# Kernel optimization log

Hardware: AMD Instinct MI355X
Metric: run time of the kernel (lower is better)

Reference implementation:

```python
import jax, jax.numpy as jnp
import numpy as np

B, T, D = 2, 2048, 2048
H = 16
DK = 64          # head_k_dim (key_dim = D*0.5 = 1024)
DV = 128         # head_v_dim (value_dim = D*1.0 = 2048)
R = 16           # gate_low_rank_dim
GLN = 16.0       # gate_logit_normalizer
C = 64           # chunk size
EPS = 1e-5


def setup_inputs() -> dict:
    key = jax.random.key(0)
    ks = jax.random.split(key, 12)
    s = 0.02
    return {
        "hidden_states": jax.random.normal(ks[0], (B, T, D), jnp.float32),
        "Wq": jax.random.normal(ks[1], (D, H * DK), jnp.float32) * s,
        "Wk": jax.random.normal(ks[2], (D, H * DK), jnp.float32) * s,
        "Wv": jax.random.normal(ks[3], (D, H * DV), jnp.float32) * s,
        "Wgk1": jax.random.normal(ks[4], (D, R), jnp.float32) * s,
        "Wgk2": jax.random.normal(ks[5], (R, H * DK), jnp.float32) * s,
        "bgk2": jnp.zeros((H * DK,), jnp.float32),
        "Wg1": jax.random.normal(ks[6], (D, R), jnp.float32) * s,
        "Wg2": jax.random.normal(ks[7], (R, H * DV), jnp.float32) * s,
        "bg2": jnp.zeros((H * DV,), jnp.float32),
        "Wo": jax.random.normal(ks[8], (H * DV, D), jnp.float32) * s,
        "gnorm_w": jnp.ones((DV,), jnp.float32),
    }


def _gla_chunk(q, k, v, gk):
    """Chunked gated linear attention.
    q,k,gk: [B,T,H,DK], v: [B,T,H,DV]. Recurrence:
    S_t = diag(exp(gk_t)) S_{t-1} + k_t v_t^T ; o_t = q_t @ S_t.
    """
    nC = T // C
    # [nC, B, H, C, d]
    def to_chunks(x):
        return x.reshape(B, nC, C, H, -1).transpose(1, 0, 3, 2, 4)
    qc, kc, vc, gkc = map(to_chunks, (q, k, v, gk))
    Gc = jnp.cumsum(gkc, axis=3)  # inclusive cumsum of log-decays within chunk
    tri = jnp.tril(jnp.ones((C, C), bool))

    def step(S, inp):
        q_c, k_c, v_c, G_c = inp  # [B,H,C,dk] / [B,H,C,dv]
        qg = q_c * jnp.exp(G_c)            # decays <= 0 within chunk -> safe
        kg = k_c * jnp.exp(-G_c)
        # inter-chunk: state contribution
        o = jnp.einsum('bhcd,bhde->bhce', qg, S)
        # intra-chunk causal attention with decay
        A = jnp.einsum('bhid,bhjd->bhij', qg, kg)
        A = jnp.where(tri, A, 0.0)
        o = o + jnp.einsum('bhij,bhje->bhie', A, v_c)
        # state update
        G_last = G_c[:, :, -1, :]                       # [B,H,dk]
        k_dec = k_c * jnp.exp(G_last[:, :, None, :] - G_c)
        S = S * jnp.exp(G_last)[:, :, :, None] + jnp.einsum('bhcd,bhce->bhde', k_dec, v_c)
        return S, o

    S0 = jnp.zeros((B, H, DK, DV), q.dtype)
    _, o = jax.lax.scan(step, S0, (qc, kc, vc, Gc))
    # [nC,B,H,C,dv] -> [B,T,H,dv]
    return o.transpose(1, 0, 3, 2, 4).reshape(B, T, H, DV)


def reference(hidden_states, Wq, Wk, Wv, Wgk1, Wgk2, bgk2, Wg1, Wg2, bg2, Wo, gnorm_w):
    hs = hidden_states
    q = jax.nn.silu(hs @ Wq).reshape(B, T, H, DK)
    k = jax.nn.silu(hs @ Wk).reshape(B, T, H, DK)
    v = jax.nn.silu(hs @ Wv).reshape(B, T, H, DV)
    gk = ((hs @ Wgk1) @ Wgk2 + bgk2).reshape(B, T, H, DK)
    gk = jax.nn.log_sigmoid(gk) / GLN
    q = q * (DK ** -0.5)  # fla default scale
    o = _gla_chunk(q, k, v, gk)  # [B,T,H,DV]
    # RMSNorm over head_v_dim
    o = o * jax.lax.rsqrt(jnp.mean(o * o, axis=-1, keepdims=True) + EPS) * gnorm_w
    g = ((hs @ Wg1) @ Wg2 + bg2).reshape(B, T, H, DV)
    o = o * jax.nn.sigmoid(g)
    return o.reshape(B, T, H * DV) @ Wo
```

## Files before the change

kernel.cpp:

```cpp
#include <hip/hip_runtime.h>
#include <cstdint>

#define Bq   2
#define Tq   2048
#define Dq   2048
#define Hq   16
#define DKq  64
#define DVq  128
#define Cq   64
#define NCq  32
#define Mq   4096
#define NBH  32

typedef _Float16 f16;
typedef f16 f16x4 __attribute__((ext_vector_type(4)));
typedef f16 f16x8 __attribute__((ext_vector_type(8)));
typedef float f32x4 __attribute__((ext_vector_type(4)));
typedef unsigned short u16;
typedef u16 u16x8 __attribute__((ext_vector_type(8)));

__device__ __forceinline__ void gl_lds16(const void* g, void* l) {
    __builtin_amdgcn_global_load_lds(
        (const __attribute__((address_space(1))) uint32_t*)g,
        (__attribute__((address_space(3))) uint32_t*)l, 16, 0, 0);
}

__global__ __launch_bounds__(256) void trans_all(const float* __restrict__ Wq,
                                                 const float* __restrict__ Wk,
                                                 const float* __restrict__ Wv,
                                                 const float* __restrict__ Wo,
                                                 f16* __restrict__ Qkv, f16* __restrict__ WoT) {
    __shared__ float sh[4096];
    int blk = blockIdx.x;
    int tid = threadIdx.x;
    const float* W; f16* Dh; int N, nt, kt; long rowoff;
    if (blk < 2048)      { W = Wq; N = 1024; int t = blk;        nt = t & 31; kt = t >> 5; Dh = Qkv; rowoff = 0; }
    else if (blk < 4096) { W = Wk; N = 1024; int t = blk - 2048; nt = t & 31; kt = t >> 5; Dh = Qkv; rowoff = 1024; }
    else if (blk < 8192) { W = Wv; N = 2048; int t = blk - 4096; nt = t & 63; kt = t >> 6; Dh = Qkv; rowoff = 2048; }
    else                 { W = Wo; N = 2048; int t = blk - 8192; nt = t & 63; kt = t >> 6; Dh = WoT; rowoff = 0; }
    int tx = tid & 31, ty = tid >> 5;
#pragma unroll
    for (int i = 0; i < 4; i++) {
        int k = kt * 32 + ty + i * 8;
        int n = nt * 32 + tx;
        sh[tx * 33 + ty + i * 8] = W[(long)k * N + n];
    }
    __syncthreads();
#pragma unroll
    for (int i = 0; i < 4; i++) {
        int n = nt * 32 + ty + i * 8;
        int k = kt * 32 + tx;
        Dh[(rowoff + n) * 2048L + k] = (f16)sh[(ty + i * 8) * 33 + tx];
    }
}

__global__ __launch_bounds__(256) void hs_conv(const float* __restrict__ in,
                                               f16* __restrict__ out) {
    long i = ((long)blockIdx.x * 256 + threadIdx.x) * 8;
    float4 a = *(const float4*)(in + i);
    float4 b = *(const float4*)(in + i + 4);
    f16x8 h;
    h[0] = (f16)a.x; h[1] = (f16)a.y; h[2] = (f16)a.z; h[3] = (f16)a.w;
    h[4] = (f16)b.x; h[5] = (f16)b.y; h[6] = (f16)b.z; h[7] = (f16)b.w;
    *(f16x8*)(out + i) = h;
}

__global__ __launch_bounds__(256) void lowrank_tg(const float* __restrict__ hs,
                                                  const float* __restrict__ Wgk1,
                                                  const float* __restrict__ Wg1,
                                                  float* __restrict__ t_gk,
                                                  float* __restrict__ t_g) {
    __shared__ float sW[512 * 32];
    int tid = threadIdx.x;
    int blk = blockIdx.x;
    int r = tid >> 4, seg = tid & 15;
    long row = (long)blk * 16 + r;
    float acc[32];
#pragma unroll
    for (int c = 0; c < 32; c++) acc[c] = 0.f;
    for (int kc = 0; kc < 2048; kc += 512) {
        __syncthreads();
#pragma unroll
        for (int i = 0; i < 16; i++) {
            int s = tid + i * 256;
            int k = s >> 3, q = s & 7;
            float4 w = (q < 4) ? *(const float4*)(Wgk1 + (long)(kc + k) * 16 + q * 4)
                               : *(const float4*)(Wg1  + (long)(kc + k) * 16 + (q - 4) * 4);
            int qs = q ^ ((k >> 5) & 7);
            *(float4*)&sW[k * 32 + qs * 4] = w;
        }
        __syncthreads();
        const float* hp = hs + row * 2048 + kc + seg * 32;
        int xr = seg & 7;
#pragma unroll
        for (int k4 = 0; k4 < 8; k4++) {
            float4 hv = *(const float4*)(hp + k4 * 4);
            float hvv[4] = {hv.x, hv.y, hv.z, hv.w};
#pragma unroll
            for (int u = 0; u < 4; u++) {
                int k = seg * 32 + k4 * 4 + u;
                const float* wr = &sW[k * 32];
#pragma unroll
                for (int q = 0; q < 8; q++) {
                    float4 wv = *(const float4*)(wr + ((q ^ xr) * 4));
                    acc[q * 4 + 0] += hvv[u] * wv.x;
                    acc[q * 4 + 1] += hvv[u] * wv.y;
                    acc[q * 4 + 2] += hvv[u] * wv.z;
                    acc[q * 4 + 3] += hvv[u] * wv.w;
                }
            }
        }
    }
#pragma unroll
    for (int c = 0; c < 32; c++) {
        acc[c] += __shfl_xor(acc[c], 1);
        acc[c] += __shfl_xor(acc[c], 2);
        acc[c] += __shfl_xor(acc[c], 4);
        acc[c] += __shfl_xor(acc[c], 8);
    }
    if (seg == 0) {
        float4 a;
        a.x = acc[0];  a.y = acc[1];  a.z = acc[2];  a.w = acc[3];  *(float4*)(t_gk + row * 16)     = a;
        a.x = acc[4];  a.y = acc[5];  a.z = acc[6];  a.w = acc[7];  *(float4*)(t_gk + row * 16 + 4) = a;
        a.x = acc[8];  a.y = acc[9];  a.z = acc[10]; a.w = acc[11]; *(float4*)(t_gk + row * 16 + 8) = a;
        a.x = acc[12]; a.y = acc[13]; a.z = acc[14]; a.w = acc[15]; *(float4*)(t_gk + row * 16 + 12)= a;
        a.x = acc[16]; a.y = acc[17]; a.z = acc[18]; a.w = acc[19]; *(float4*)(t_g + row * 16)      = a;
        a.x = acc[20]; a.y = acc[21]; a.z = acc[22]; a.w = acc[23]; *(float4*)(t_g + row * 16 + 4)  = a;
        a.x = acc[24]; a.y = acc[25]; a.z = acc[26]; a.w = acc[27]; *(float4*)(t_g + row * 16 + 8)  = a;
        a.x = acc[28]; a.y = acc[29]; a.z = acc[30]; a.w = acc[31]; *(float4*)(t_g + row * 16 + 12) = a;
    }
}

#define BARX()   asm volatile("s_barrier" ::: "memory")
#define LGKM0()  asm volatile("s_waitcnt lgkmcnt(0)" ::: "memory")
#define VMW8()   asm volatile("s_waitcnt vmcnt(8)" ::: "memory")

__global__ __launch_bounds__(512, 2) void gemm256(const f16* __restrict__ A,
                                                  const f16* __restrict__ Bt,
                                                  float* __restrict__ o0,
                                                  f16* __restrict__ h0,
                                                  f16* __restrict__ h1,
                                                  f16* __restrict__ h2,
                                                  int mode) {
    __shared__ __align__(16) f16 sA[2][16384];
    __shared__ __align__(16) f16 sB[2][16384];
    int tid = threadIdx.x;
    int wave = tid >> 6, lane = tid & 63;
    int quad = lane >> 4, l16 = lane & 15;
    int wm = wave >> 2, wn = wave & 3;

    int cpx = (int)gridDim.x >> 3;
    int wid = ((int)blockIdx.x & 7) * cpx + ((int)blockIdx.x >> 3);
    int bm = wid & 15, bn = wid >> 4;

    const f16* Ab = A  + (long)bm * 256 * 2048;
    const f16* Bb = Bt + (long)bn * 256 * 2048;

    int srow = tid >> 3;
    int gsrc = ((tid & 7) ^ (srow & 7)) * 8;
    const f16* Asrc = Ab + (long)srow * 2048 + gsrc;
    const f16* Bsrc = Bb + (long)srow * 2048 + gsrc;

#define STAGE(P, KT) do { \
    const f16* as_ = Asrc + (KT) * 64; \
    const f16* bs_ = Bsrc + (KT) * 64; \
    f16* la_ = &sA[P][tid * 8]; \
    f16* lb_ = &sB[P][tid * 8]; \
    _Pragma("unroll") \
    for (int q_ = 0; q_ < 4; q_++) gl_lds16(as_ + (long)q_ * 64 * 2048, la_ + q_ * 4096); \
    _Pragma("unroll") \
    for (int q_ = 0; q_ < 4; q_++) gl_lds16(bs_ + (long)q_ * 64 * 2048, lb_ + q_ * 4096); \
} while (0)

    int go0 = (quad ^ (l16 & 7)) * 8;
    int go1 = go0 ^ 32;
    const f16* aB0 = &sA[0][(wm * 128 + l16) * 64];
    const f16* aB1 = &sA[1][(wm * 128 + l16) * 64];
    const f16* bB0 = &sB[0][(wn * 64 + l16) * 64];
    const f16* bB1 = &sB[1][(wn * 64 + l16) * 64];

    f16x8 afr[4][2], bfr[2][2][2];
    f32x4 acc[8][4] = {};

#define LDA(PB, MH) do { \
    _Pragma("unroll") \
    for (int ii_ = 0; ii_ < 4; ii_++) { \
        afr[ii_][0] = *(const f16x8*)(PB + ((MH) * 4 + ii_) * 1024 + go0); \
        afr[ii_][1] = *(const f16x8*)(PB + ((MH) * 4 + ii_) * 1024 + go1); \
    } \
} while (0)

#define LDB(PB, NH) do { \
    _Pragma("unroll") \
    for (int jj_ = 0; jj_ < 2; jj_++) { \
        bfr[NH][jj_][0] = *(const f16x8*)(PB + ((NH) * 2 + jj_) * 1024 + go0); \
        bfr[NH][jj_][1] = *(const f16x8*)(PB + ((NH) * 2 + jj_) * 1024 + go1); \
    } \
} while (0)

#define QMFMA(MH, NH) do { \
    __builtin_amdgcn_s_setprio(1); \
    _Pragma("unroll") \
    for (int ii_ = 0; ii_ < 4; ii_++) \
    _Pragma("unroll") \
    for (int jj_ = 0; jj_ < 2; jj_++) { \
        acc[(MH)*4+ii_][(NH)*2+jj_] = __builtin_amdgcn_mfma_f32_16x16x32_f16(afr[ii_][0], bfr[NH][jj_][0], acc[(MH)*4+ii_][(NH)*2+jj_], 0, 0, 0); \
        acc[(MH)*4+ii_][(NH)*2+jj_] = __builtin_amdgcn_mfma_f32_16x16x32_f16(afr[ii_][1], bfr[NH][jj_][1], acc[(MH)*4+ii_][(NH)*2+jj_], 0, 0, 0); \
    } \
    __builtin_amdgcn_s_setprio(0); \
} while (0)

    STAGE(0, 0);
    STAGE(1, 1);
    VMW8();
    BARX();

#pragma unroll 1
    for (int it = 0; it < 16; it++) {
        int kt2 = 2 * it + 2; if (kt2 > 31) kt2 = 31;
        int kt3 = 2 * it + 3; if (kt3 > 31) kt3 = 31;
        LDA(aB0, 0); LDB(bB0, 0);
        BARX(); LGKM0(); QMFMA(0, 0); BARX();
        LDB(bB0, 1);
        BARX(); LGKM0(); QMFMA(0, 1); BARX();
        LDA(aB0, 1);
        BARX(); LGKM0(); QMFMA(1, 0); BARX();
        STAGE(0, kt2);
        VMW8();
        BARX(); QMFMA(1, 1); BARX();
        LDA(aB1, 0); LDB(bB1, 0);
        BARX(); LGKM0(); QMFMA(0, 0); BARX();
        LDB(bB1, 1);
        BARX(); LGKM0(); QMFMA(0, 1); BARX();
        LDA(aB1, 1);
        BARX(); LGKM0(); QMFMA(1, 0); BARX();
        STAGE(1, kt3);
        VMW8();
        BARX(); QMFMA(1, 1); BARX();
    }
    asm volatile("s_waitcnt vmcnt(0)" ::: "memory");

    long rb = (long)bm * 256 + wm * 128 + quad * 4;
    if (mode == 0) {
        long cbase = (long)bn * 256 + wn * 64 + l16;
#pragma unroll
        for (int i = 0; i < 8; i++)
#pragma unroll
            for (int j = 0; j < 4; j++)
#pragma unroll
                for (int r = 0; r < 4; r++)
                    o0[(rb + i * 16 + r) * 2048 + cbase + j * 16] = acc[i][j][r];
    } else {
        f16* dst; long cw, cb; float sc = 1.f;
        if (bn < 4)      { dst = h0; cw = 1024; cb = (long)bn * 256;       sc = 0.125f; }
        else if (bn < 8) { dst = h1; cw = 1024; cb = (long)(bn - 4) * 256; }
        else             { dst = h2; cw = 2048; cb = (long)(bn - 8) * 256; }
        long cbase = cb + wn * 64 + l16;
#pragma unroll
        for (int i = 0; i < 8; i++)
#pragma unroll
            for (int j = 0; j < 4; j++)
#pragma unroll
                for (int r = 0; r < 4; r++) {
                    float x = acc[i][j][r];
                    x = x / (1.f + __expf(-x)) * sc;
                    dst[(rb + i * 16 + r) * cw + cbase + j * 16] = (f16)x;
                }
    }
#undef STAGE
#undef LDA
#undef LDB
#undef QMFMA
}

__global__ __launch_bounds__(256) void vtrans(const u16* __restrict__ v,
                                              u16* __restrict__ vT) {
    __shared__ uint32_t su[128 * 65];
    int tid = threadIdx.x;
    int t0 = (blockIdx.x >> 5) * 128;
    int e0 = (blockIdx.x & 31) * 64;
#pragma unroll
    for (int i = 0; i < 4; i++) {
        int tr = i * 32 + (tid >> 3);
        int ec = (tid & 7) * 8;
        u16x8 g = *(const u16x8*)(v + (long)(t0 + tr) * 2048 + e0 + ec);
#pragma unroll
        for (int j = 0; j < 8; j++) su[tr * 65 + ec + j] = g[j];
    }
    __syncthreads();
#pragma unroll
    for (int i = 0; i < 2; i++) {
        int er = i * 32 + (tid >> 3);
        int tch = (tid & 7) * 16;
        u16x8 o0, o1;
#pragma unroll
        for (int j = 0; j < 8; j++) {
            o0[j] = (u16)su[(tch + j) * 65 + er];
            o1[j] = (u16)su[(tch + 8 + j) * 65 + er];
        }
        u16* dst = vT + (long)(e0 + er) * 4096 + t0 + tch;
        *(u16x8*)dst = o0;
        *(u16x8*)(dst + 8) = o1;
    }
}

__global__ __launch_bounds__(256) void gk_cum(const float* __restrict__ t_gk,
                                              const float* __restrict__ Wgk2,
                                              const float* __restrict__ bgk2,
                                              float* __restrict__ G,
                                              float* __restrict__ dec) {
    __shared__ float sT[1024];
    __shared__ float sW[1024];
    __shared__ float sb[64];
    __shared__ float sG[64 * 64];
    int blk = blockIdx.x;
    int c = blk & 31, h = (blk >> 5) & 15, b = blk >> 9;
    int tid = threadIdx.x;
    long rowbase = (long)b * Tq + c * 64;
    {
        int idx = tid * 4;
        *(float4*)&sT[idx] = *(const float4*)(t_gk + rowbase * 16 + idx);
        int rr = idx >> 6, dd = idx & 63;
        *(float4*)&sW[idx] = *(const float4*)(Wgk2 + rr * 1024 + h * 64 + dd);
    }
    if (tid < 64) sb[tid] = bgk2[h * 64 + tid];
    __syncthreads();
    int tquad = tid >> 4, dgrp = tid & 15;
    float4 bg4 = *(float4*)&sb[dgrp * 4];
#pragma unroll
    for (int j = 0; j < 4; j++) {
        int t = tquad * 4 + j;
        float4 z = bg4;
#pragma unroll
        for (int rr = 0; rr < 16; rr++) {
            float tv = sT[t * 16 + rr];
            float4 wv = *(float4*)&sW[rr * 64 + dgrp * 4];
            z.x += tv * wv.x; z.y += tv * wv.y; z.z += tv * wv.z; z.w += tv * wv.w;
        }
        float4 o;
        o.x = (fminf(z.x, 0.f) - log1pf(__expf(-fabsf(z.x)))) * 0.0625f;
        o.y = (fminf(z.y, 0.f) - log1pf(__expf(-fabsf(z.y)))) * 0.0625f;
        o.z = (fminf(z.z, 0.f) - log1pf(__expf(-fabsf(z.z)))) * 0.0625f;
        o.w = (fminf(z.w, 0.f) - log1pf(__expf(-fabsf(z.w)))) * 0.0625f;
        *(float4*)&sG[t * 64 + dgrp * 4] = o;
    }
    __syncthreads();
    if (tid < 64) {
        float run = 0.f;
        for (int t = 0; t < 64; t++) { run += sG[t * 64 + tid]; sG[t * 64 + tid] = run; }
        dec[blk * 64 + tid] = __expf(run);
    }
    __syncthreads();
    float* Gb = G + (long)blk * 4096;
#pragma unroll
    for (int i = 0; i < 4; i++) {
        int f = tid + i * 256;
        *(float4*)(Gb + f * 4) = *(float4*)&sG[f * 4];
    }
}

#define ST 68
__global__ __launch_bounds__(256) void gla_pass1(const f16* __restrict__ kbuf,
                                                 const f16* __restrict__ vh,
                                                 const float* __restrict__ G,
                                                 float* __restrict__ U) {
    __shared__ float sG[64 * ST];
    __shared__ float sK[64 * ST];
    int blk = blockIdx.x;
    int c = blk & 31, h = (blk >> 5) & 15, b = blk >> 9;
    int tid = threadIdx.x;
    long rowbase = (long)b * Tq + c * 64;
    const float* Gb = G + (long)blk * 4096;
#pragma unroll
    for (int i = 0; i < 4; i++) {
        int f = tid + i * 256;
        float4 v = *(const float4*)(Gb + f * 4);
        int t = f >> 4, d0 = (f & 15) * 4;
        *(float4*)&sG[t * ST + d0] = v;
    }
    __syncthreads();
#pragma unroll
    for (int i = 0; i < 16; i++) {
        int idx = tid + i * 256;
        int t = idx >> 6, d = idx & 63;
        float gl = sG[63 * ST + d];
        sK[t * ST + d] = (float)kbuf[(rowbase + t) * 1024 + h * 64 + d] * __expf(gl - sG[t * ST + d]);
    }
    __syncthreads();
    int ty = tid >> 4, tx = tid & 15;
    float acc[4][8] = {};
    const f16* vb = vh + rowbase * 2048 + h * 128 + tx * 8;
    for (int t = 0; t < 64; t++) {
        float kd[4];
        *(float4*)&kd[0] = *(float4*)&sK[t * ST + ty * 4];
        f16x8 vv = *(const f16x8*)(vb + (long)t * 2048);
        float ve[8];
#pragma unroll
        for (int e = 0; e < 8; e++) ve[e] = (float)vv[e];
#pragma unroll
        for (int r = 0; r < 4; r++)
#pragma unroll
            for (int e = 0; e < 8; e++) acc[r][e] += kd[r] * ve[e];
    }
    float* Ub = U + (long)blk * 8192;
#pragma unroll
    for (int r = 0; r < 4; r++) {
        int d = ty * 4 + r;
#pragma unroll
        for (int e8 = 0; e8 < 8; e8++)
            Ub[(tx * 8 + e8) * 64 + d] = acc[r][e8];
    }
}

__global__ __launch_bounds__(256) void gla_pass2(const float* __restrict__ U,
                                                 const float* __restrict__ dec,
                                                 f16* __restrict__ ShT) {
    int bh = blockIdx.x >> 2;
    int tid = threadIdx.x;
    int e = (blockIdx.x & 3) * 32 + (tid >> 3);
    int d0 = (tid & 7) * 8;
    float4 Sa = {0.f, 0.f, 0.f, 0.f}, Sb = {0.f, 0.f, 0.f, 0.f};
    for (int c = 0; c < NCq; c++) {
        long base = ((long)(bh * 32 + c) * 128 + e) * 64 + d0;
        float4 u0 = *(const float4*)(U + base);
        float4 u1 = *(const float4*)(U + base + 4);
        const float* dp = dec + (bh * 32 + c) * 64 + d0;
        float4 dc0 = *(const float4*)dp;
        float4 dc1 = *(const float4*)(dp + 4);
        f16x8 sh;
        sh[0] = (f16)Sa.x; sh[1] = (f16)Sa.y; sh[2] = (f16)Sa.z; sh[3] = (f16)Sa.w;
        sh[4] = (f16)Sb.x; sh[5] = (f16)Sb.y; sh[6] = (f16)Sb.z; sh[7] = (f16)Sb.w;
        *(f16x8*)(ShT + base) = sh;
        Sa.x = Sa.x * dc0.x + u0.x; Sa.y = Sa.y * dc0.y + u0.y;
        Sa.z = Sa.z * dc0.z + u0.z; Sa.w = Sa.w * dc0.w + u0.w;
        Sb.x = Sb.x * dc1.x + u1.x; Sb.y = Sb.y * dc1.y + u1.y;
        Sb.z = Sb.z * dc1.z + u1.z; Sb.w = Sb.w * dc1.w + u1.w;
    }
}

#define GRD(row, kslot) (((row) << 6) + ((((kslot) ^ ((row) & 7))) << 3))
__global__ __launch_bounds__(256) void gla_pass3(const f16* __restrict__ qb,
                                                 const f16* __restrict__ kb,
                                                 const float* __restrict__ G,
                                                 const float* __restrict__ t_g,
                                                 const float* __restrict__ Wg2,
                                                 const float* __restrict__ bg2,
                                                 const float* __restrict__ gnw,
                                                 const f16* __restrict__ ShT,
                                                 const f16* __restrict__ vT,
                                                 f16* __restrict__ Oh) {
    __shared__ __align__(16) f16 sQg[4096];
    __shared__ __align__(16) f16 sKg[4096];
    __shared__ __align__(16) f16 sAh[4096];
    __shared__ __align__(16) f16 sST[8192];
    __shared__ __align__(16) f16 sVT[8192];
    __shared__ float sWg[16 * 128];
    __shared__ float sbg[128];
    int blk = blockIdx.x;
    int c = blk & 31, h = (blk >> 5) & 15, b = blk >> 9;
    int tid = threadIdx.x;
    long rowbase = (long)b * Tq + c * 64;

#pragma unroll
    for (int i = 0; i < 4; i++) {
        int s = tid + i * 256;
        int e = s >> 3, gp = s & 7;
        int gl = gp ^ (e & 7);
        gl_lds16(ShT + (long)blk * 8192 + e * 64 + gl * 8, sST + s * 8);
        gl_lds16(vT + (long)(h * 128 + e) * 4096 + rowbase + gl * 8, sVT + s * 8);
    }
#pragma unroll
    for (int i = 0; i < 2; i++) {
        int idx = tid * 4 + i * 1024;
        int rr = idx >> 7, ee = idx & 127;
        *(float4*)&sWg[idx] = *(const float4*)(Wg2 + (long)rr * 2048 + h * 128 + ee);
    }
    if (tid < 128) sbg[tid] = bg2[h * 128 + tid];
#pragma unroll
    for (int i = 0; i < 4; i++) {
        int f = tid + i * 256;
        int t = f >> 4, gi = f & 15;
        float4 G4 = *(const float4*)(G + (long)blk * 4096 + f * 4);
        long gb = (rowbase + t) * 1024 + h * 64 + gi * 4;
        f16x4 q4 = *(const f16x4*)(qb + gb);
        f16x4 k4 = *(const f16x4*)(kb + gb);
        f16x4 qh, kh;
        float ex;
        ex = __expf(G4.x); qh[0] = (f16)((float)q4[0] * ex); kh[0] = (f16)((float)k4[0] / ex);
        ex = __expf(G4.y); qh[1] = (f16)((float)q4[1] * ex); kh[1] = (f16)((float)k4[1] / ex);
        ex = __expf(G4.z); qh[2] = (f16)((float)q4[2] * ex); kh[2] = (f16)((float)k4[2] / ex);
        ex = __expf(G4.w); qh[3] = (f16)((float)q4[3] * ex); kh[3] = (f16)((float)k4[3] / ex);
        int w = (t << 6) + ((((gi >> 1) ^ (t & 7))) << 3) + ((gi & 1) << 2);
        *(f16x4*)(sQg + w) = qh;
        *(f16x4*)(sKg + w) = kh;
    }
    __syncthreads();

    int wv = tid >> 6, lane = tid & 63;
    int quad = lane >> 4, l16 = lane & 15;
    int trow = wv * 16 + l16;

    f16x8 afq[2];
    afq[0] = *(const f16x8*)(sQg + GRD(trow, quad));
    afq[1] = *(const f16x8*)(sQg + GRD(trow, 4 + quad));
#pragma unroll
    for (int j4 = 0; j4 < 4; j4++) {
        int tc = j4 * 16 + l16;
        f16x8 bk0 = *(const f16x8*)(sKg + GRD(tc, quad));
        f16x8 bk1 = *(const f16x8*)(sKg + GRD(tc, 4 + quad));
        f32x4 ca = {};
        ca = __builtin_amdgcn_mfma_f32_16x16x32_f16(afq[0], bk0, ca, 0, 0, 0);
        ca = __builtin_amdgcn_mfma_f32_16x16x32_f16(afq[1], bk1, ca, 0, 0, 0);
#pragma unroll
        for (int r = 0; r < 4; r++) {
            int tr = wv * 16 + quad * 4 + r;
            int tcw = j4 * 16 + l16;
            f16 av = (tcw <= tr) ? (f16)ca[r] : (f16)0.f;
            sAh[(tr << 6) + ((((tcw >> 3) ^ (tr & 7))) << 3) + (tcw & 7)] = av;
        }
    }

    f16x8 afa[2];
    afa[0] = *(const f16x8*)(sAh + GRD(trow, quad));
    afa[1] = *(const f16x8*)(sAh + GRD(trow, 4 + quad));
    f32x4 acc[8];
#pragma unroll
    for (int et = 0; et < 8; et++) {
        int e = et * 16 + l16;
        f16x8 bs0 = *(const f16x8*)(sST + GRD(e, quad));
        f16x8 bs1 = *(const f16x8*)(sST + GRD(e, 4 + quad));
        f16x8 bv0 = *(const f16x8*)(sVT + GRD(e, quad));
        f16x8 bv1 = *(const f16x8*)(sVT + GRD(e, 4 + quad));
        f32x4 cc = {};
        cc = __builtin_amdgcn_mfma_f32_16x16x32_f16(afq[0], bs0, cc, 0, 0, 0);
        cc = __builtin_amdgcn_mfma_f32_16x16x32_f16(afq[1], bs1, cc, 0, 0, 0);
        cc = __builtin_amdgcn_mfma_f32_16x16x32_f16(afa[0], bv0, cc, 0, 0, 0);
        cc = __builtin_amdgcn_mfma_f32_16x16x32_f16(afa[1], bv1, cc, 0, 0, 0);
        acc[et] = cc;
    }

    float gw[8], bgv[8];
#pragma unroll
    for (int et = 0; et < 8; et++) {
        gw[et]  = gnw[et * 16 + l16];
        bgv[et] = sbg[et * 16 + l16];
    }
#pragma unroll
    for (int half = 0; half < 2; half++) {
        float tg[2][16];
#pragma unroll
        for (int rh = 0; rh < 2; rh++) {
            int t = wv * 16 + quad * 4 + half * 2 + rh;
            const float* tgp = t_g + (rowbase + t) * 16;
#pragma unroll
            for (int q4 = 0; q4 < 4; q4++)
                *(float4*)&tg[rh][q4 * 4] = *(const float4*)(tgp + q4 * 4);
        }
        float g[2][8];
#pragma unroll
        for (int rh = 0; rh < 2; rh++)
#pragma unroll
            for (int et = 0; et < 8; et++) g[rh][et] = bgv[et];
#pragma unroll
        for (int rr = 0; rr < 16; rr++) {
#pragma unroll
            for (int et = 0; et < 8; et++) {
                float wv_ = sWg[rr * 128 + et * 16 + l16];
                g[0][et] += tg[0][rr] * wv_;
                g[1][et] += tg[1][rr] * wv_;
            }
        }
#pragma unroll
        for (int rh = 0; rh < 2; rh++) {
            int r = half * 2 + rh;
            int t = wv * 16 + quad * 4 + r;
            float ss = 0.f;
#pragma unroll
            for (int et = 0; et < 8; et++) ss += acc[et][r] * acc[et][r];
            ss += __shfl_xor(ss, 1);
            ss += __shfl_xor(ss, 2);
            ss += __shfl_xor(ss, 4);
            ss += __shfl_xor(ss, 8);
            float scale = rsqrtf(ss * (1.f / 128.f) + 1e-5f);
            long off = (rowbase + t) * 2048 + h * 128 + l16;
#pragma unroll
            for (int et = 0; et < 8; et++) {
                float y = acc[et][r] * scale * gw[et] / (1.f + __expf(-g[rh][et]));
                Oh[off + et * 16] = (f16)y;
            }
        }
    }
}

extern "C" void kernel_launch(void* const* d_in, const int* in_sizes, int n_in,
                              void* d_out, int out_size, void* d_ws, size_t ws_size,
                              hipStream_t stream) {
    const float* hs   = (const float*)d_in[0];
    const float* Wq   = (const float*)d_in[1];
    const float* Wk   = (const float*)d_in[2];
    const float* Wv   = (const float*)d_in[3];
    const float* Wgk1 = (const float*)d_in[4];
    const float* Wgk2 = (const float*)d_in[5];
    const float* bgk2 = (const float*)d_in[6];
    const float* Wg1  = (const float*)d_in[7];
    const float* Wg2  = (const float*)d_in[8];
    const float* bg2  = (const float*)d_in[9];
    const float* Wo   = (const float*)d_in[10];
    const float* gnw  = (const float*)d_in[11];

    char* w = (char*)d_ws;
    auto alloc = [&](size_t bytes) {
        char* p = w; w += (bytes + 255) & ~size_t(255); return (void*)p;
    };
    f16*   Xh     = (f16*)  alloc((size_t)Mq * Dq * 2);
    f16*   WqkvT  = (f16*)  alloc((size_t)4224 * 2048 * 2);
    f16*   WoT    = (f16*)  alloc((size_t)2048 * 2048 * 2);
    f16*   qb     = (f16*)  alloc((size_t)Mq * 1024 * 2);
    f16*   kb     = (f16*)  alloc((size_t)Mq * 1024 * 2);
    f16*   vhb    = (f16*)  alloc((size_t)Mq * 2048 * 2);
    f16*   vTb    = (f16*)  alloc((size_t)Mq * 2048 * 2);
    float* t_gk   = (float*)alloc((size_t)Mq * 16 * 4);
    float* t_g    = (float*)alloc((size_t)Mq * 16 * 4);
    float* Ut     = (float*)alloc((size_t)NBH * NCq * 8192 * 4);
    f16*   ShT    = (f16*)  alloc((size_t)NBH * NCq * 8192 * 2);
    float* dec    = (float*)alloc((size_t)NBH * NCq * 64 * 4);
    float* Gbuf   = (float*)alloc((size_t)NBH * NCq * 4096 * 4);

    trans_all<<<12288, 256, 0, stream>>>(Wq, Wk, Wv, Wo, WqkvT, WoT);
    hs_conv<<<Mq * Dq / 2048, 256, 0, stream>>>(hs, Xh);
    lowrank_tg<<<256, 256, 0, stream>>>(hs, Wgk1, Wg1, t_gk, t_g);

    gemm256<<<256, 512, 0, stream>>>(Xh, WqkvT, nullptr, qb, kb, vhb, 1);
    vtrans<<<1024, 256, 0, stream>>>((const u16*)vhb, (u16*)vTb);

    gk_cum<<<NBH * NCq, 256, 0, stream>>>(t_gk, Wgk2, bgk2, Gbuf, dec);
    gla_pass1<<<NBH * NCq, 256, 0, stream>>>(kb, vhb, Gbuf, Ut);
    gla_pass2<<<NBH * 4, 256, 0, stream>>>(Ut, dec, ShT);
    gla_pass3<<<NBH * NCq, 256, 0, stream>>>(qb, kb, Gbuf, t_g, Wg2, bg2, gnw, ShT, vTb, Xh);

    gemm256<<<128, 512, 0, stream>>>(Xh, WoT, (float*)d_out, nullptr, nullptr, nullptr, 0);
}
```

Before: 415.2 us.

## Shrink GEMM tile to 128x256 with register double-buffered fragment pipeline

The gemm256 kernel's per-block tile changes from 256x256 to 128x256, which doubles the grid for both the QKV projection and the output projection. The output GEMM now launches 256 blocks instead of 128, filling more compute units. The inner loop is rebuilt so that LDS fragment reads for the next K-step are issued into a second register set while MFMAs run on the current one, with far fewer barriers per iteration. In exchange, each block reuses each B tile across fewer rows of A, so the kernel loads more data in total.

```diff
diff --git a/kernel.cpp b/kernel.cpp
--- a/kernel.cpp
+++ b/kernel.cpp
@@ -133,7 +133,7 @@
 
 #define BARX()   asm volatile("s_barrier" ::: "memory")
 #define LGKM0()  asm volatile("s_waitcnt lgkmcnt(0)" ::: "memory")
-#define VMW8()   asm volatile("s_waitcnt vmcnt(8)" ::: "memory")
+#define VMW6()   asm volatile("s_waitcnt vmcnt(6)" ::: "memory")
 
 __global__ __launch_bounds__(512, 2) void gemm256(const f16* __restrict__ A,
                                                   const f16* __restrict__ Bt,
@@ -142,8 +142,8 @@
                                                   f16* __restrict__ h1,
                                                   f16* __restrict__ h2,
                                                   int mode) {
-    __shared__ __align__(16) f16 sA[2][16384];
-    __shared__ __align__(16) f16 sB[2][16384];
+    __shared__ __align__(16) f16 sAb[16384];
+    __shared__ __align__(16) f16 sBb[32768];
     int tid = threadIdx.x;
     int wave = tid >> 6, lane = tid & 63;
     int quad = lane >> 4, l16 = lane & 15;
@@ -151,105 +151,90 @@
 
     int cpx = (int)gridDim.x >> 3;
     int wid = ((int)blockIdx.x & 7) * cpx + ((int)blockIdx.x >> 3);
-    int bm = wid & 15, bn = wid >> 4;
-
-    const f16* Ab = A  + (long)bm * 256 * 2048;
-    const f16* Bb = Bt + (long)bn * 256 * 2048;
+    int bm = wid & 31, bn = wid >> 5;
 
     int srow = tid >> 3;
     int gsrc = ((tid & 7) ^ (srow & 7)) * 8;
-    const f16* Asrc = Ab + (long)srow * 2048 + gsrc;
-    const f16* Bsrc = Bb + (long)srow * 2048 + gsrc;
+    const f16* Asrc = A  + ((long)bm * 128 + srow) * 2048 + gsrc;
+    const f16* Bsrc = Bt + ((long)bn * 256 + srow) * 2048 + gsrc;
 
 #define STAGE(P, KT) do { \
-    const f16* as_ = Asrc + (KT) * 64; \
-    const f16* bs_ = Bsrc + (KT) * 64; \
-    f16* la_ = &sA[P][tid * 8]; \
-    f16* lb_ = &sB[P][tid * 8]; \
     _Pragma("unroll") \
-    for (int q_ = 0; q_ < 4; q_++) gl_lds16(as_ + (long)q_ * 64 * 2048, la_ + q_ * 4096); \
+    for (int q_ = 0; q_ < 2; q_++) \
+        gl_lds16(Asrc + (KT) * 64 + (long)q_ * 64 * 2048, sAb + (P) * 8192 + tid * 8 + q_ * 4096); \
     _Pragma("unroll") \
-    for (int q_ = 0; q_ < 4; q_++) gl_lds16(bs_ + (long)q_ * 64 * 2048, lb_ + q_ * 4096); \
+    for (int q_ = 0; q_ < 4; q_++) \
+        gl_lds16(Bsrc + (KT) * 64 + (long)q_ * 64 * 2048, sBb + (P) * 16384 + tid * 8 + q_ * 4096); \
 } while (0)
 
     int go0 = (quad ^ (l16 & 7)) * 8;
     int go1 = go0 ^ 32;
-    const f16* aB0 = &sA[0][(wm * 128 + l16) * 64];
-    const f16* aB1 = &sA[1][(wm * 128 + l16) * 64];
-    const f16* bB0 = &sB[0][(wn * 64 + l16) * 64];
-    const f16* bB1 = &sB[1][(wn * 64 + l16) * 64];
-
-    f16x8 afr[4][2], bfr[2][2][2];
-    f32x4 acc[8][4] = {};
-
-#define LDA(PB, MH) do { \
-    _Pragma("unroll") \
-    for (int ii_ = 0; ii_ < 4; ii_++) { \
-        afr[ii_][0] = *(const f16x8*)(PB + ((MH) * 4 + ii_) * 1024 + go0); \
-        afr[ii_][1] = *(const f16x8*)(PB + ((MH) * 4 + ii_) * 1024 + go1); \
-    } \
+    const f16* pA0 = sAb + (wm * 64 + l16) * 64 + go0;
+    const f16* pA1 = sAb + (wm * 64 + l16) * 64 + go1;
+    const f16* pB0 = sBb + (wn * 64 + l16) * 64 + go0;
+    const f16* pB1 = sBb + (wn * 64 + l16) * 64 + go1;
+
+    f16x8 aX[4], bX[4], aY[4], bY[4];
+    f32x4 acc[4][4] = {};
+
+#define RDA(D, PTR, POFF) do { \
+    D[0] = *(const f16x8*)((PTR) + (POFF)); \
+    D[1] = *(const f16x8*)((PTR) + (POFF) + 1024); \
+    D[2] = *(const f16x8*)((PTR) + (POFF) + 2048); \
+    D[3] = *(const f16x8*)((PTR) + (POFF) + 3072); \
 } while (0)
 
-#define LDB(PB, NH) do { \
-    _Pragma("unroll") \
-    for (int jj_ = 0; jj_ < 2; jj_++) { \
-        bfr[NH][jj_][0] = *(const f16x8*)(PB + ((NH) * 2 + jj_) * 1024 + go0); \
-        bfr[NH][jj_][1] = *(const f16x8*)(PB + ((NH) * 2 + jj_) * 1024 + go1); \
-    } \
-} while (0)
-
-#define QMFMA(MH, NH) do { \
+#define MM(AS, BS) do { \
     __builtin_amdgcn_s_setprio(1); \
     _Pragma("unroll") \
-    for (int ii_ = 0; ii_ < 4; ii_++) \
+    for (int m_ = 0; m_ < 4; m_++) \
     _Pragma("unroll") \
-    for (int jj_ = 0; jj_ < 2; jj_++) { \
-        acc[(MH)*4+ii_][(NH)*2+jj_] = __builtin_amdgcn_mfma_f32_16x16x32_f16(afr[ii_][0], bfr[NH][jj_][0], acc[(MH)*4+ii_][(NH)*2+jj_], 0, 0, 0); \
-        acc[(MH)*4+ii_][(NH)*2+jj_] = __builtin_amdgcn_mfma_f32_16x16x32_f16(afr[ii_][1], bfr[NH][jj_][1], acc[(MH)*4+ii_][(NH)*2+jj_], 0, 0, 0); \
-    } \
+    for (int n_ = 0; n_ < 4; n_++) \
+        acc[m_][n_] = __builtin_amdgcn_mfma_f32_16x16x32_f16(AS[m_], BS[n_], acc[m_][n_], 0, 0, 0); \
     __builtin_amdgcn_s_setprio(0); \
 } while (0)
 
     STAGE(0, 0);
     STAGE(1, 1);
-    VMW8();
+    VMW6();
     BARX();
+    RDA(aX, pA0, 0); RDA(bX, pB0, 0);
 
 #pragma unroll 1
     for (int it = 0; it < 16; it++) {
-        int kt2 = 2 * it + 2; if (kt2 > 31) kt2 = 31;
-        int kt3 = 2 * it + 3; if (kt3 > 31) kt3 = 31;
-        LDA(aB0, 0); LDB(bB0, 0);
-        BARX(); LGKM0(); QMFMA(0, 0); BARX();
-        LDB(bB0, 1);
-        BARX(); LGKM0(); QMFMA(0, 1); BARX();
-        LDA(aB0, 1);
-        BARX(); LGKM0(); QMFMA(1, 0); BARX();
-        STAGE(0, kt2);
-        VMW8();
-        BARX(); QMFMA(1, 1); BARX();
-        LDA(aB1, 0); LDB(bB1, 0);
-        BARX(); LGKM0(); QMFMA(0, 0); BARX();
-        LDB(bB1, 1);
-        BARX(); LGKM0(); QMFMA(0, 1); BARX();
-        LDA(aB1, 1);
-        BARX(); LGKM0(); QMFMA(1, 0); BARX();
-        STAGE(1, kt3);
-        VMW8();
-        BARX(); QMFMA(1, 1); BARX();
+        int c2 = 2 * it + 2; if (c2 > 31) c2 = 31;
+        int c3 = 2 * it + 3; if (c3 > 31) c3 = 31;
+        RDA(aY, pA1, 0); RDA(bY, pB1, 0);
+        MM(aX, bX);
+        LGKM0();
+        BARX();
+        STAGE(0, c2);
+        VMW6();
+        BARX();
+        RDA(aX, pA0, 8192); RDA(bX, pB0, 16384);
+        MM(aY, bY);
+        RDA(aY, pA1, 8192); RDA(bY, pB1, 16384);
+        MM(aX, bX);
+        LGKM0();
+        BARX();
+        STAGE(1, c3);
+        VMW6();
+        BARX();
+        RDA(aX, pA0, 0); RDA(bX, pB0, 0);
+        MM(aY, bY);
     }
     asm volatile("s_waitcnt vmcnt(0)" ::: "memory");
 
-    long rb = (long)bm * 256 + wm * 128 + quad * 4;
+    long rb = (long)bm * 128 + wm * 64 + quad * 4;
     if (mode == 0) {
         long cbase = (long)bn * 256 + wn * 64 + l16;
 #pragma unroll
-        for (int i = 0; i < 8; i++)
-#pragma unroll
-            for (int j = 0; j < 4; j++)
+        for (int m = 0; m < 4; m++)
+#pragma unroll
+            for (int n = 0; n < 4; n++)
 #pragma unroll
                 for (int r = 0; r < 4; r++)
-                    o0[(rb + i * 16 + r) * 2048 + cbase + j * 16] = acc[i][j][r];
+                    o0[(rb + m * 16 + r) * 2048 + cbase + n * 16] = acc[m][n][r];
     } else {
         f16* dst; long cw, cb; float sc = 1.f;
         if (bn < 4)      { dst = h0; cw = 1024; cb = (long)bn * 256;       sc = 0.125f; }
@@ -257,20 +242,19 @@
         else             { dst = h2; cw = 2048; cb = (long)(bn - 8) * 256; }
         long cbase = cb + wn * 64 + l16;
 #pragma unroll
-        for (int i = 0; i < 8; i++)
-#pragma unroll
-            for (int j = 0; j < 4; j++)
+        for (int m = 0; m < 4; m++)
+#pragma unroll
+            for (int n = 0; n < 4; n++)
 #pragma unroll
                 for (int r = 0; r < 4; r++) {
-                    float x = acc[i][j][r];
+                    float x = acc[m][n][r];
                     x = x / (1.f + __expf(-x)) * sc;
-                    dst[(rb + i * 16 + r) * cw + cbase + j * 16] = (f16)x;
+                    dst[(rb + m * 16 + r) * cw + cbase + n * 16] = (f16)x;
                 }
     }
 #undef STAGE
-#undef LDA
-#undef LDB
-#undef QMFMA
+#undef RDA
+#undef MM
 }
 
 __global__ __launch_bounds__(256) void vtrans(const u16* __restrict__ v,
@@ -630,7 +614,7 @@
     hs_conv<<<Mq * Dq / 2048, 256, 0, stream>>>(hs, Xh);
     lowrank_tg<<<256, 256, 0, stream>>>(hs, Wgk1, Wg1, t_gk, t_g);
 
-    gemm256<<<256, 512, 0, stream>>>(Xh, WqkvT, nullptr, qb, kb, vhb, 1);
+    gemm256<<<512, 512, 0, stream>>>(Xh, WqkvT, nullptr, qb, kb, vhb, 1);
     vtrans<<<1024, 256, 0, stream>>>((const u16*)vhb, (u16*)vTb);
 
     gk_cum<<<NBH * NCq, 256, 0, stream>>>(t_gk, Wgk2, bgk2, Gbuf, dec);
@@ -638,5 +622,5 @@
     gla_pass2<<<NBH * 4, 256, 0, stream>>>(Ut, dec, ShT);
     gla_pass3<<<NBH * NCq, 256, 0, stream>>>(qb, kb, Gbuf, t_g, Wg2, bg2, gnw, ShT, vTb, Xh);
 
-    gemm256<<<128, 512, 0, stream>>>(Xh, WoT, (float*)d_out, nullptr, nullptr, nullptr, 0);
-}
+    gemm256<<<256, 512, 0, stream>>>(Xh, WoT, (float*)d_out, nullptr, nullptr, nullptr, 0);
+}
```

Measured after the change: 419.9 us. About the same (+1.1%).

## Split output GEMM into dedicated 128x256-tile kernel to fill all CUs

Applied to the files above, without the earlier changes.

The shared gemm256 kernel is split into a QKV-only variant and a new output-projection kernel, gemm128o, which uses 128x256 tiles. With smaller M tiles the output GEMM launches 256 blocks instead of 128, so more of the GPU's compute units have work for the final projection. The new kernel has its own double-buffered LDS pipeline with register ping-pong of MFMA operands and raised wave priority around the MFMA blocks. Each block now holds less output per unit of traffic, so A/B reuse is lower and more loads are issued per FLOP.

```diff
diff --git a/kernel.cpp b/kernel.cpp
--- a/kernel.cpp
+++ b/kernel.cpp
@@ -24,6 +24,11 @@
         (const __attribute__((address_space(1))) uint32_t*)g,
         (__attribute__((address_space(3))) uint32_t*)l, 16, 0, 0);
 }
+
+#define BARX()   asm volatile("s_barrier" ::: "memory")
+#define LGKM0()  asm volatile("s_waitcnt lgkmcnt(0)" ::: "memory")
+#define VMW8()   asm volatile("s_waitcnt vmcnt(8)" ::: "memory")
+#define VMW6()   asm volatile("s_waitcnt vmcnt(6)" ::: "memory")
 
 __global__ __launch_bounds__(256) void trans_all(const float* __restrict__ Wq,
                                                  const float* __restrict__ Wk,
@@ -131,17 +136,11 @@
     }
 }
 
-#define BARX()   asm volatile("s_barrier" ::: "memory")
-#define LGKM0()  asm volatile("s_waitcnt lgkmcnt(0)" ::: "memory")
-#define VMW8()   asm volatile("s_waitcnt vmcnt(8)" ::: "memory")
-
-__global__ __launch_bounds__(512, 2) void gemm256(const f16* __restrict__ A,
-                                                  const f16* __restrict__ Bt,
-                                                  float* __restrict__ o0,
-                                                  f16* __restrict__ h0,
-                                                  f16* __restrict__ h1,
-                                                  f16* __restrict__ h2,
-                                                  int mode) {
+__global__ __launch_bounds__(512, 2) void gemm256q(const f16* __restrict__ A,
+                                                   const f16* __restrict__ Bt,
+                                                   f16* __restrict__ h0,
+                                                   f16* __restrict__ h1,
+                                                   f16* __restrict__ h2) {
     __shared__ __align__(16) f16 sA[2][16384];
     __shared__ __align__(16) f16 sB[2][16384];
     int tid = threadIdx.x;
@@ -241,36 +240,125 @@
     asm volatile("s_waitcnt vmcnt(0)" ::: "memory");
 
     long rb = (long)bm * 256 + wm * 128 + quad * 4;
-    if (mode == 0) {
-        long cbase = (long)bn * 256 + wn * 64 + l16;
-#pragma unroll
-        for (int i = 0; i < 8; i++)
-#pragma unroll
-            for (int j = 0; j < 4; j++)
-#pragma unroll
-                for (int r = 0; r < 4; r++)
-                    o0[(rb + i * 16 + r) * 2048 + cbase + j * 16] = acc[i][j][r];
-    } else {
-        f16* dst; long cw, cb; float sc = 1.f;
-        if (bn < 4)      { dst = h0; cw = 1024; cb = (long)bn * 256;       sc = 0.125f; }
-        else if (bn < 8) { dst = h1; cw = 1024; cb = (long)(bn - 4) * 256; }
-        else             { dst = h2; cw = 2048; cb = (long)(bn - 8) * 256; }
-        long cbase = cb + wn * 64 + l16;
-#pragma unroll
-        for (int i = 0; i < 8; i++)
-#pragma unroll
-            for (int j = 0; j < 4; j++)
-#pragma unroll
-                for (int r = 0; r < 4; r++) {
-                    float x = acc[i][j][r];
-                    x = x / (1.f + __expf(-x)) * sc;
-                    dst[(rb + i * 16 + r) * cw + cbase + j * 16] = (f16)x;
-                }
-    }
+    f16* dst; long cw, cb; float sc = 1.f;
+    if (bn < 4)      { dst = h0; cw = 1024; cb = (long)bn * 256;       sc = 0.125f; }
+    else if (bn < 8) { dst = h1; cw = 1024; cb = (long)(bn - 4) * 256; }
+    else             { dst = h2; cw = 2048; cb = (long)(bn - 8) * 256; }
+    long cbase = cb + wn * 64 + l16;
+#pragma unroll
+    for (int i = 0; i < 8; i++)
+#pragma unroll
+        for (int j = 0; j < 4; j++)
+#pragma unroll
+            for (int r = 0; r < 4; r++) {
+                float x = acc[i][j][r];
+                x = x / (1.f + __expf(-x)) * sc;
+                dst[(rb + i * 16 + r) * cw + cbase + j * 16] = (f16)x;
+            }
 #undef STAGE
 #undef LDA
 #undef LDB
 #undef QMFMA
+}
+
+__global__ __launch_bounds__(512, 2) void gemm128o(const f16* __restrict__ A,
+                                                   const f16* __restrict__ Bt,
+                                                   float* __restrict__ o0) {
+    __shared__ __align__(16) f16 sAb[16384];
+    __shared__ __align__(16) f16 sBb[32768];
+    int tid = threadIdx.x;
+    int wave = tid >> 6, lane = tid & 63;
+    int quad = lane >> 4, l16 = lane & 15;
+    int wm = wave >> 2, wn = wave & 3;
+
+    int cpx = (int)gridDim.x >> 3;
+    int wid = ((int)blockIdx.x & 7) * cpx + ((int)blockIdx.x >> 3);
+    int bm = wid & 31, bn = wid >> 5;
+
+    int srow = tid >> 3;
+    int gsrc = ((tid & 7) ^ (srow & 7)) * 8;
+    const f16* Asrc = A  + ((long)bm * 128 + srow) * 2048 + gsrc;
+    const f16* Bsrc = Bt + ((long)bn * 256 + srow) * 2048 + gsrc;
+
+#define STAGE(P, KT) do { \
+    _Pragma("unroll") \
+    for (int q_ = 0; q_ < 2; q_++) \
+        gl_lds16(Asrc + (KT) * 64 + (long)q_ * 64 * 2048, sAb + (P) * 8192 + tid * 8 + q_ * 4096); \
+    _Pragma("unroll") \
+    for (int q_ = 0; q_ < 4; q_++) \
+        gl_lds16(Bsrc + (KT) * 64 + (long)q_ * 64 * 2048, sBb + (P) * 16384 + tid * 8 + q_ * 4096); \
+} while (0)
+
+    int go0 = (quad ^ (l16 & 7)) * 8;
+    int go1 = go0 ^ 32;
+    const f16* pA0 = sAb + (wm * 64 + l16) * 64 + go0;
+    const f16* pA1 = sAb + (wm * 64 + l16) * 64 + go1;
+    const f16* pB0 = sBb + (wn * 64 + l16) * 64 + go0;
+    const f16* pB1 = sBb + (wn * 64 + l16) * 64 + go1;
+
+    f16x8 aX[4], bX[4], aY[4], bY[4];
+    f32x4 acc[4][4] = {};
+
+#define RDA(D, PTR, POFF) do { \
+    D[0] = *(const f16x8*)((PTR) + (POFF)); \
+    D[1] = *(const f16x8*)((PTR) + (POFF) + 1024); \
+    D[2] = *(const f16x8*)((PTR) + (POFF) + 2048); \
+    D[3] = *(const f16x8*)((PTR) + (POFF) + 3072); \
+} while (0)
+
+#define MM(AS, BS) do { \
+    __builtin_amdgcn_s_setprio(1); \
+    _Pragma("unroll") \
+    for (int m_ = 0; m_ < 4; m_++) \
+    _Pragma("unroll") \
+    for (int n_ = 0; n_ < 4; n_++) \
+        acc[m_][n_] = __builtin_amdgcn_mfma_f32_16x16x32_f16(AS[m_], BS[n_], acc[m_][n_], 0, 0, 0); \
+    __builtin_amdgcn_s_setprio(0); \
+} while (0)
+
+    STAGE(0, 0);
+    STAGE(1, 1);
+    VMW6();
+    BARX();
+    RDA(aX, pA0, 0); RDA(bX, pB0, 0);
+
+#pragma unroll 1
+    for (int it = 0; it < 16; it++) {
+        int c2 = 2 * it + 2; if (c2 > 31) c2 = 31;
+        int c3 = 2 * it + 3; if (c3 > 31) c3 = 31;
+        RDA(aY, pA1, 0); RDA(bY, pB1, 0);
+        MM(aX, bX);
+        LGKM0();
+        BARX();
+        STAGE(0, c2);
+        VMW6();
+        BARX();
+        RDA(aX, pA0, 8192); RDA(bX, pB0, 16384);
+        MM(aY, bY);
+        RDA(aY, pA1, 8192); RDA(bY, pB1, 16384);
+        MM(aX, bX);
+        LGKM0();
+        BARX();
+        STAGE(1, c3);
+        VMW6();
+        BARX();
+        RDA(aX, pA0, 0); RDA(bX, pB0, 0);
+        MM(aY, bY);
+    }
+    asm volatile("s_waitcnt vmcnt(0)" ::: "memory");
+
+    long rb = (long)bm * 128 + wm * 64 + quad * 4;
+    long cbase = (long)bn * 256 + wn * 64 + l16;
+#pragma unroll
+    for (int m = 0; m < 4; m++)
+#pragma unroll
+        for (int n = 0; n < 4; n++)
+#pragma unroll
+            for (int r = 0; r < 4; r++)
+                o0[(rb + m * 16 + r) * 2048 + cbase + n * 16] = acc[m][n][r];
+#undef STAGE
+#undef RDA
+#undef MM
 }
 
 __global__ __launch_bounds__(256) void vtrans(const u16* __restrict__ v,
@@ -630,7 +718,7 @@
     hs_conv<<<Mq * Dq / 2048, 256, 0, stream>>>(hs, Xh);
     lowrank_tg<<<256, 256, 0, stream>>>(hs, Wgk1, Wg1, t_gk, t_g);
 
-    gemm256<<<256, 512, 0, stream>>>(Xh, WqkvT, nullptr, qb, kb, vhb, 1);
+    gemm256q<<<256, 512, 0, stream>>>(Xh, WqkvT, qb, kb, vhb);
     vtrans<<<1024, 256, 0, stream>>>((const u16*)vhb, (u16*)vTb);
 
     gk_cum<<<NBH * NCq, 256, 0, stream>>>(t_gk, Wgk2, bgk2, Gbuf, dec);
@@ -638,5 +726,5 @@
     gla_pass2<<<NBH * 4, 256, 0, stream>>>(Ut, dec, ShT);
     gla_pass3<<<NBH * NCq, 256, 0, stream>>>(qb, kb, Gbuf, t_g, Wg2, bg2, gnw, ShT, vTb, Xh);
 
-    gemm256<<<128, 512, 0, stream>>>(Xh, WoT, (float*)d_out, nullptr, nullptr, nullptr, 0);
-}
+    gemm128o<<<256, 512, 0, stream>>>(Xh, WoT, (float*)d_out);
+}
```

Result: faster. 396.6 us (-4.5%).
